# Performance work log

Hardware: AMD Instinct MI355X
Metric: run time of the kernel (lower is better)

Reference implementation:

```python
import jax, jax.numpy as jnp
import numpy as np

N_NODES = 50000
N_EDGES = 800000
D_IN = 128
D_HID = 128
D_OUT = 128


def setup_inputs() -> dict:
    key = jax.random.key(0)
    ks = jax.random.split(key, 12)
    features = jax.random.normal(ks[0], (N_NODES, D_IN), dtype=jnp.float32)
    src = jax.random.randint(ks[1], (N_EDGES,), 0, N_NODES, dtype=jnp.int32)
    dst = jax.random.randint(ks[2], (N_EDGES,), 0, N_NODES, dtype=jnp.int32)
    s_in = 1.0 / np.sqrt(D_IN)
    s_hid = 1.0 / np.sqrt(D_HID)
    W1 = jax.random.normal(ks[3], (D_IN, D_HID), dtype=jnp.float32) * s_in
    b1 = jnp.zeros((D_HID,), dtype=jnp.float32)
    W2 = jax.random.normal(ks[4], (D_HID, D_HID), dtype=jnp.float32) * s_hid
    b2 = jnp.zeros((D_HID,), dtype=jnp.float32)
    W3 = jax.random.normal(ks[5], (D_HID, D_OUT), dtype=jnp.float32) * s_hid
    b3 = jnp.zeros((D_OUT,), dtype=jnp.float32)
    policy_w = jax.random.normal(ks[6], (D_OUT, 1), dtype=jnp.float32) * s_hid
    policy_b = jnp.zeros((1,), dtype=jnp.float32)
    value_w = jax.random.normal(ks[7], (D_OUT, 1), dtype=jnp.float32) * s_hid
    value_b = jnp.zeros((1,), dtype=jnp.float32)
    return {
        "features": features, "src": src, "dst": dst,
        "W1": W1, "b1": b1, "W2": W2, "b2": b2, "W3": W3, "b3": b3,
        "policy_w": policy_w, "policy_b": policy_b,
        "value_w": value_w, "value_b": value_b,
    }


def _graph_conv(h, src, dst, deg_inv, W, b, act):
    # DGL GraphConv with norm='left': scale source features by 1/out_degree,
    # sum messages over incoming edges, then linear transform + bias (+ act).
    hn = h * deg_inv  # [N, d]
    agg = jax.ops.segment_sum(hn[src], dst, num_segments=N_NODES)  # SpMM: [N, d]
    out = agg @ W + b
    return jax.nn.relu(out) if act else out


def reference(features, src, dst, W1, b1, W2, b2, W3, b3,
              policy_w, policy_b, value_w, value_b):
    ones = jnp.ones((src.shape[0],), dtype=features.dtype)
    deg = jax.ops.segment_sum(ones, src, num_segments=N_NODES)  # out-degree
    deg_inv = (1.0 / jnp.clip(deg, 1.0))[:, None]  # [N, 1]

    h = _graph_conv(features, src, dst, deg_inv, W1, b1, act=True)
    h = _graph_conv(h, src, dst, deg_inv, W2, b2, act=True)
    h = _graph_conv(h, src, dst, deg_inv, W3, b3, act=False)  # last layer: no activation

    mN = jnp.mean(h, axis=0, keepdims=True)  # mean readout over nodes, [1, D_OUT]
    PI = h @ policy_w + policy_b  # [N, 1]
    V = mN @ value_w + value_b    # [1, 1]
    return PI, V
```

## Files before the change

### kernel.cpp

```cpp
#include <hip/hip_runtime.h>


#define N_NODES 50000
#define N_EDGES 800000
#define D 128
#define NSH 8
#define PROWS (N_NODES + 8)
#define PANEL ((size_t)PROWS * 16)
#define NC 64
#define CSZ (N_EDGES / NC)
#define NW (N_NODES / 2)
#define RQH 4
#define NWQ (NW / RQH)
#define CS_CAP (N_EDGES + 8 * N_NODES)
#define TROWS 80


__global__ __launch_bounds__(512) void k_hist3(const int* __restrict__ src, const int* __restrict__ dst,
                                               unsigned* __restrict__ ghd16, unsigned* __restrict__ ghs16) {
    __shared__ unsigned h[NWQ];
    const int rq  = blockIdx.x & 3;
    const int arr = (blockIdx.x >> 2) & 1;
    const int c   = blockIdx.x >> 3;
    const int wbase = rq * NWQ;
    const int nbase = wbase * 2;
    const int t = threadIdx.x;
    for (int i = t; i < NWQ; i += 512) h[i] = 0u;
    __syncthreads();
    const int* __restrict__ col = arr ? src : dst;
    const int e0 = c * CSZ, e1 = e0 + CSZ;
    for (int e = e0 + t; e < e1; e += 512) {
        unsigned loc = (unsigned)(col[e] - nbase);
        if (loc < 2u * NWQ) atomicAdd(&h[loc >> 1], 1u << ((loc & 1) << 4));
    }
    __syncthreads();
    unsigned* __restrict__ outp = (arr ? ghs16 : ghd16) + (size_t)c * NW + wbase;
    for (int i = t; i < NWQ; i += 512) outp[i] = h[i];
}

__global__ __launch_bounds__(256) void k_merge3(unsigned* __restrict__ ghd16, const unsigned* __restrict__ ghs16,
                                                int* __restrict__ rowcnt, int* __restrict__ rowtrue,
                                                float* __restrict__ dinv) {
    int w = blockIdx.x * 256 + threadIdx.x;
    if (w >= NW) return;
    unsigned runlo = 0, runhi = 0;
#pragma unroll
    for (int c = 0; c < NC; c++) {
        unsigned v = ghd16[(size_t)c * NW + w];
        ghd16[(size_t)c * NW + w] = runlo | (runhi << 16);
        runlo += v & 0xffffu; runhi += v >> 16;
    }
    rowtrue[2 * w]     = (int)runlo;
    rowtrue[2 * w + 1] = (int)runhi;
    rowcnt[2 * w]      = (int)((runlo + 7u) & ~7u);
    rowcnt[2 * w + 1]  = (int)((runhi + 7u) & ~7u);
    unsigned dlo = 0, dhi = 0;
#pragma unroll
    for (int c = 0; c < NC; c++) {
        unsigned v = ghs16[(size_t)c * NW + w];
        dlo += v & 0xffffu; dhi += v >> 16;
    }
    dinv[2 * w]     = 1.0f / (float)(dlo > 1u ? dlo : 1u);
    dinv[2 * w + 1] = 1.0f / (float)(dhi > 1u ? dhi : 1u);
}

__global__ __launch_bounds__(1024) void k_scan1(const int* __restrict__ cnt, int* __restrict__ excl,
                                                int* __restrict__ blocksum, int n) {
    __shared__ int wsum[16];
    int i = blockIdx.x * 1024 + threadIdx.x;
    int v = (i < n) ? cnt[i] : 0;
    int lane = threadIdx.x & 63, wid = threadIdx.x >> 6;
    int x = v;
#pragma unroll
    for (int off = 1; off < 64; off <<= 1) {
        int y = __shfl_up(x, off, 64);
        if (lane >= off) x += y;
    }
    if (lane == 63) wsum[wid] = x;
    __syncthreads();
    if (threadIdx.x == 0) {
        int run = 0;
        for (int w = 0; w < 16; w++) { int t = wsum[w]; wsum[w] = run; run += t; }
        blocksum[blockIdx.x] = run;
    }
    __syncthreads();
    if (i < n) excl[i] = (x - v) + wsum[wid];
}

__global__ void k_scan2(const int* __restrict__ blocksum, int* __restrict__ blockoff,
                        int* __restrict__ rowptr_last, int nblk) {
    if (threadIdx.x == 0) {
        int run = 0;
        for (int b = 0; b < nblk; b++) { int t = blocksum[b]; blockoff[b] = run; run += t; }
        rowptr_last[0] = run;
    }
}

__global__ __launch_bounds__(1024) void k_scan3(int* __restrict__ excl, const int* __restrict__ blockoff, int n) {
    int i = blockIdx.x * 1024 + threadIdx.x;
    if (i < n) excl[i] += blockoff[blockIdx.x];
}

__global__ __launch_bounds__(512) void k_fill3(const int* __restrict__ src, const int* __restrict__ dst,
                                               const int* __restrict__ rowptr, const unsigned* __restrict__ ghd16,
                                               unsigned short* __restrict__ cs16) {
    __shared__ unsigned cnt[NWQ];
    const int rq = blockIdx.x & 3;
    const int c  = blockIdx.x >> 2;
    const int nbase = rq * NWQ * 2;
    const int t = threadIdx.x;
    for (int i = t; i < NWQ; i += 512) cnt[i] = 0u;
    __syncthreads();
    const unsigned* __restrict__ basep = ghd16 + (size_t)c * NW;
    const int e0 = c * CSZ, e1 = e0 + CSZ;
    for (int e = e0 + t; e < e1; e += 512) {
        int d = dst[e];
        unsigned loc = (unsigned)(d - nbase);
        if (loc < 2u * NWQ) {
            int sh = (loc & 1) << 4;
            unsigned old = atomicAdd(&cnt[loc >> 1], 1u << sh);
            int p = (int)((old >> sh) & 0xffffu);
            int base = (int)((basep[d >> 1] >> ((d & 1) << 4)) & 0xffffu);
            cs16[rowptr[d] + base + p] = (unsigned short)src[e];
        }
    }
}

__global__ __launch_bounds__(256) void k_pad(const int* __restrict__ rowptr, const int* __restrict__ rowtrue,
                                             unsigned short* __restrict__ cs16,
                                             float* __restrict__ bufA, float* __restrict__ bufB) {
    int n = blockIdx.x * 256 + threadIdx.x;
    if (n < N_NODES) {
        int e0 = rowptr[n] + rowtrue[n], e1 = rowptr[n + 1];
        for (int e = e0; e < e1; e++) cs16[e] = (unsigned short)N_NODES;
    }
    if (blockIdx.x == 0) {
        int t = threadIdx.x;
        float* b = (t & 128) ? bufB : bufA;
        int p = (t >> 4) & 7, cc = t & 15;
        b[(size_t)p * PANEL + (size_t)N_NODES * 16 + cc] = 0.f;
    }
}


__global__ __launch_bounds__(256) void k_panelize(const float* __restrict__ in, const float* __restrict__ dinv,
                                                  float* __restrict__ outp) {
    int tid = blockIdx.x * 256 + threadIdx.x;
    if (tid >= N_NODES * 32) return;
    int p = tid / (N_NODES * 4);
    int r = tid - p * (N_NODES * 4);
    int node = r >> 2, qq = r & 3;
    float w = dinv[node];
    float4 v = *reinterpret_cast<const float4*>(&in[(size_t)node * D + p * 16 + qq * 4]);
    v.x *= w; v.y *= w; v.z *= w; v.w *= w;
    *reinterpret_cast<float4*>(&outp[(size_t)p * PANEL + (size_t)node * 16 + qq * 4]) = v;
}


__global__ __launch_bounds__(256) void k_agg(const float* __restrict__ hp,
                                             const int* __restrict__ rp, const unsigned short* __restrict__ cs16,
                                             float* __restrict__ outp) {
    const int l4 = threadIdx.x & 3;
    const int grp = threadIdx.x >> 2;
    const int slice = blockIdx.x & (NSH - 1);
    const int node = (blockIdx.x >> 3) * 64 + grp;
    if (node >= N_NODES) return;
    const float* __restrict__ pan = hp + (size_t)slice * PANEL + l4 * 4;
    int s0 = rp[node], s1 = rp[node + 1];
    float4 acc = {0.f, 0.f, 0.f, 0.f};
    for (int e = s0; e < s1; e += 8) {
        int4 r = *reinterpret_cast<const int4*>(&cs16[e]);
        int i0 = r.x & 0xffff, i1 = (r.x >> 16) & 0xffff;
        int i2 = r.y & 0xffff, i3 = (r.y >> 16) & 0xffff;
        int i4 = r.z & 0xffff, i5 = (r.z >> 16) & 0xffff;
        int i6 = r.w & 0xffff, i7 = (r.w >> 16) & 0xffff;
        float4 a0 = *reinterpret_cast<const float4*>(&pan[(size_t)i0 * 16]);
        float4 a1 = *reinterpret_cast<const float4*>(&pan[(size_t)i1 * 16]);
        float4 a2 = *reinterpret_cast<const float4*>(&pan[(size_t)i2 * 16]);
        float4 a3 = *reinterpret_cast<const float4*>(&pan[(size_t)i3 * 16]);
        float4 a4 = *reinterpret_cast<const float4*>(&pan[(size_t)i4 * 16]);
        float4 a5 = *reinterpret_cast<const float4*>(&pan[(size_t)i5 * 16]);
        float4 a6 = *reinterpret_cast<const float4*>(&pan[(size_t)i6 * 16]);
        float4 a7 = *reinterpret_cast<const float4*>(&pan[(size_t)i7 * 16]);
        acc.x += ((a0.x + a1.x) + (a2.x + a3.x)) + ((a4.x + a5.x) + (a6.x + a7.x));
        acc.y += ((a0.y + a1.y) + (a2.y + a3.y)) + ((a4.y + a5.y) + (a6.y + a7.y));
        acc.z += ((a0.z + a1.z) + (a2.z + a3.z)) + ((a4.z + a5.z) + (a6.z + a7.z));
        acc.w += ((a0.w + a1.w) + (a2.w + a3.w)) + ((a4.w + a5.w) + (a6.w + a7.w));
    }
    *reinterpret_cast<float4*>(&outp[(size_t)slice * PANEL + (size_t)node * 16 + l4 * 4]) = acc;
}


__global__ __launch_bounds__(256, 3) void k_gemm(const float* __restrict__ in, const float* __restrict__ W,
                                                 const float* __restrict__ bias, float* __restrict__ out,
                                                 int nrows, int relu,
                                                 const float* __restrict__ dscale,
                                                 const float* __restrict__ pw, const float* __restrict__ pb,
                                                 float* __restrict__ pi_out, float* __restrict__ colsum) {
    __shared__ float wl[64 * D];
    __shared__ float at[64 * TROWS];
    int t = threadIdx.x;
    const int head = (pw != nullptr);
    const int tx = t & 15;
    const int ro = t >> 4;
    const int row0 = blockIdx.x * TROWS;
    float4 bv1 = reinterpret_cast<const float4*>(bias)[tx];
    float4 bv2 = reinterpret_cast<const float4*>(bias)[16 + tx];
    float4 pw1 = head ? reinterpret_cast<const float4*>(pw)[tx]      : float4{0, 0, 0, 0};
    float4 pw2 = head ? reinterpret_cast<const float4*>(pw)[16 + tx] : float4{0, 0, 0, 0};
    float pb0 = head ? pb[0] : 0.f;
    float4 cs1 = {0, 0, 0, 0}, cs2 = {0, 0, 0, 0};

    int sidx[5], skb[5];
#pragma unroll
    for (int j = 0; j < 5; j++) {
        int i = t + j * 256;
        int r = i % TROWS;
        int pq = i / TROWS;
        sidx[j] = r;
        skb[j] = (pq & 3) * 4 + (pq >> 2) * 16;
    }

#define LOADA(va, h)                                                                   \
    _Pragma("unroll")                                                                  \
    for (int j = 0; j < 5; j++) {                                                      \
        int i = t + j * 256;                                                           \
        int pq = i / TROWS;                                                            \
        int p = (h) * 4 + (pq >> 2);                                                   \
        int c4 = pq & 3;                                                               \
        va[j] = *reinterpret_cast<const float4*>(                                      \
            &in[(size_t)p * PANEL + (size_t)(row0 + sidx[j]) * 16 + c4 * 4]);          \
    }

#define WRITEA(va)                                                                     \
    _Pragma("unroll")                                                                  \
    for (int j = 0; j < 5; j++) {                                                      \
        int kb = skb[j], r = sidx[j];                                                  \
        at[(kb + 0) * TROWS + r] = va[j].x; at[(kb + 1) * TROWS + r] = va[j].y;        \
        at[(kb + 2) * TROWS + r] = va[j].z; at[(kb + 3) * TROWS + r] = va[j].w;        \
    }

#define STAGEW(h)                                                                      \
    _Pragma("unroll")                                                                  \
    for (int j = 0; j < 8; j++) {                                                      \
        int i = t + j * 256;                                                           \
        reinterpret_cast<float4*>(wl)[i] =                                             \
            reinterpret_cast<const float4*>(W + (h) * 64 * D)[i];                      \
    }

#define KLOOP                                                                          \
    _Pragma("unroll 4")                                                                \
    for (int kk = 0; kk < 64; kk++) {                                                  \
        float4 a  = *reinterpret_cast<const float4*>(&at[kk * TROWS + ro * 5]);        \
        float  a4 = at[kk * TROWS + ro * 5 + 4];                                       \
        float4 w1 = *reinterpret_cast<const float4*>(&wl[kk * D + tx * 4]);            \
        float4 w2 = *reinterpret_cast<const float4*>(&wl[kk * D + 64 + tx * 4]);       \
        acc[0][0] += a.x * w1.x; acc[0][1] += a.x * w1.y; acc[0][2] += a.x * w1.z; acc[0][3] += a.x * w1.w; \
        acc[0][4] += a.x * w2.x; acc[0][5] += a.x * w2.y; acc[0][6] += a.x * w2.z; acc[0][7] += a.x * w2.w; \
        acc[1][0] += a.y * w1.x; acc[1][1] += a.y * w1.y; acc[1][2] += a.y * w1.z; acc[1][3] += a.y * w1.w; \
        acc[1][4] += a.y * w2.x; acc[1][5] += a.y * w2.y; acc[1][6] += a.y * w2.z; acc[1][7] += a.y * w2.w; \
        acc[2][0] += a.z * w1.x; acc[2][1] += a.z * w1.y; acc[2][2] += a.z * w1.z; acc[2][3] += a.z * w1.w; \
        acc[2][4] += a.z * w2.x; acc[2][5] += a.z * w2.y; acc[2][6] += a.z * w2.z; acc[2][7] += a.z * w2.w; \
        acc[3][0] += a.w * w1.x; acc[3][1] += a.w * w1.y; acc[3][2] += a.w * w1.z; acc[3][3] += a.w * w1.w; \
        acc[3][4] += a.w * w2.x; acc[3][5] += a.w * w2.y; acc[3][6] += a.w * w2.z; acc[3][7] += a.w * w2.w; \
        acc[4][0] += a4 * w1.x; acc[4][1] += a4 * w1.y; acc[4][2] += a4 * w1.z; acc[4][3] += a4 * w1.w;     \
        acc[4][4] += a4 * w2.x; acc[4][5] += a4 * w2.y; acc[4][6] += a4 * w2.z; acc[4][7] += a4 * w2.w;     \
    }

    float acc[5][8];
#pragma unroll
    for (int j = 0; j < 5; j++)
#pragma unroll
        for (int c = 0; c < 8; c++) acc[j][c] = 0.f;

    float4 va[5];
    LOADA(va, 0);
    STAGEW(0);
    WRITEA(va);
    __syncthreads();
    LOADA(va, 1);
    KLOOP;
    __syncthreads();
    WRITEA(va);
    STAGEW(1);
    __syncthreads();
    KLOOP;

#pragma unroll
    for (int j = 0; j < 5; j++) {
        int gr = row0 + ro * 5 + j;
        float4 o1, o2;
        o1.x = acc[j][0] + bv1.x; o1.y = acc[j][1] + bv1.y;
        o1.z = acc[j][2] + bv1.z; o1.w = acc[j][3] + bv1.w;
        o2.x = acc[j][4] + bv2.x; o2.y = acc[j][5] + bv2.y;
        o2.z = acc[j][6] + bv2.z; o2.w = acc[j][7] + bv2.w;
        if (relu) {
            o1.x = fmaxf(o1.x, 0.f); o1.y = fmaxf(o1.y, 0.f);
            o1.z = fmaxf(o1.z, 0.f); o1.w = fmaxf(o1.w, 0.f);
            o2.x = fmaxf(o2.x, 0.f); o2.y = fmaxf(o2.y, 0.f);
            o2.z = fmaxf(o2.z, 0.f); o2.w = fmaxf(o2.w, 0.f);
        }
        if (head) {
            cs1.x += o1.x; cs1.y += o1.y; cs1.z += o1.z; cs1.w += o1.w;
            cs2.x += o2.x; cs2.y += o2.y; cs2.z += o2.z; cs2.w += o2.w;
            float pr = o1.x * pw1.x + o1.y * pw1.y + o1.z * pw1.z + o1.w * pw1.w
                     + o2.x * pw2.x + o2.y * pw2.y + o2.z * pw2.z + o2.w * pw2.w;
#pragma unroll
            for (int m = 8; m > 0; m >>= 1) pr += __shfl_xor(pr, m, 16);
            if (tx == 0) pi_out[gr] = pr + pb0;
        } else {
            if (dscale) {
                float w = dscale[gr];
                o1.x *= w; o1.y *= w; o1.z *= w; o1.w *= w;
                o2.x *= w; o2.y *= w; o2.z *= w; o2.w *= w;
            }
            size_t base1 = (size_t)(tx >> 2) * PANEL + (size_t)gr * 16 + (tx & 3) * 4;
            *reinterpret_cast<float4*>(&out[base1]) = o1;
            *reinterpret_cast<float4*>(&out[base1 + 4 * PANEL]) = o2;
        }
    }

    if (head) {
        __syncthreads();
        float* csl = at;
        if (t < D) csl[t] = 0.f;
        __syncthreads();
        atomicAdd(&csl[tx * 4 + 0], cs1.x);
        atomicAdd(&csl[tx * 4 + 1], cs1.y);
        atomicAdd(&csl[tx * 4 + 2], cs1.z);
        atomicAdd(&csl[tx * 4 + 3], cs1.w);
        atomicAdd(&csl[64 + tx * 4 + 0], cs2.x);
        atomicAdd(&csl[64 + tx * 4 + 1], cs2.y);
        atomicAdd(&csl[64 + tx * 4 + 2], cs2.z);
        atomicAdd(&csl[64 + tx * 4 + 3], cs2.w);
        __syncthreads();
        if (t < D) atomicAdd(&colsum[t], csl[t]);
    }
#undef LOADA
#undef WRITEA
#undef STAGEW
#undef KLOOP
}


__global__ __launch_bounds__(128) void k_value(const float* __restrict__ colsum, const float* __restrict__ vw,
                                               const float* __restrict__ vb, float* __restrict__ out) {
    __shared__ float red[128];
    int t = threadIdx.x;
    red[t] = (colsum[t] * (1.0f / (float)N_NODES)) * vw[t];
    __syncthreads();
    for (int s = 64; s > 0; s >>= 1) {
        if (t < s) red[t] += red[t + s];
        __syncthreads();
    }
    if (t == 0) out[0] = red[0] + vb[0];
}

__global__ __launch_bounds__(64) void k_ws_too_small(float* __restrict__ out, int n) {
    int i = blockIdx.x * 64 + threadIdx.x;
    if (i < n) out[i] = -1e30f;
}


extern "C" void kernel_launch(void* const* d_in, const int* in_sizes, int n_in,
                              void* d_out, int out_size, void* d_ws, size_t ws_size,
                              hipStream_t stream) {
    const float* features = (const float*)d_in[0];
    const int*   src      = (const int*)d_in[1];
    const int*   dst      = (const int*)d_in[2];
    const float* W1 = (const float*)d_in[3];
    const float* b1 = (const float*)d_in[4];
    const float* W2 = (const float*)d_in[5];
    const float* b2 = (const float*)d_in[6];
    const float* W3 = (const float*)d_in[7];
    const float* b3 = (const float*)d_in[8];
    const float* pw = (const float*)d_in[9];
    const float* pb = (const float*)d_in[10];
    const float* vw = (const float*)d_in[11];
    const float* vb = (const float*)d_in[12];
    float* out = (float*)d_out;

    char* ws = (char*)d_ws;
    size_t off = 0;
    auto alloc = [&](size_t bytes) -> char* {
        char* p = ws + off;
        off += (bytes + 255) & ~(size_t)255;
        return p;
    };
    float* dinv     = (float*)alloc((size_t)N_NODES * 4);
    int*   rowptr   = (int*)alloc((size_t)(N_NODES + 1) * 4);
    int*   rowcnt   = (int*)alloc((size_t)N_NODES * 4);
    int*   rowtrue  = (int*)alloc((size_t)N_NODES * 4);
    int*   blocksum = (int*)alloc(64 * 4);
    int*   blockoff = (int*)alloc(64 * 4);
    float* colsum   = (float*)alloc(D * 4);
    unsigned short* cs16 = (unsigned short*)alloc((size_t)CS_CAP * 2);
    float* bufA     = (float*)alloc((size_t)NSH * PANEL * 4);
    float* bufB     = (float*)alloc((size_t)NSH * PANEL * 4);

    unsigned* ghd16 = (unsigned*)bufB;
    unsigned* ghs16 = ghd16 + (size_t)NC * NW;

    if (off > ws_size) {
        k_ws_too_small<<<(out_size + 63) / 64, 64, 0, stream>>>(out, out_size);
        return;
    }

    hipMemsetAsync(colsum, 0, (size_t)D * 4, stream);

    k_hist3<<<NC * 2 * RQH, 512, 0, stream>>>(src, dst, ghd16, ghs16);
    k_merge3<<<(NW + 255) / 256, 256, 0, stream>>>(ghd16, ghs16, rowcnt, rowtrue, dinv);

    int nblk = (N_NODES + 1023) / 1024;
    k_scan1<<<nblk, 1024, 0, stream>>>(rowcnt, rowptr, blocksum, N_NODES);
    k_scan2<<<1, 64, 0, stream>>>(blocksum, blockoff, rowptr + N_NODES, nblk);
    k_scan3<<<nblk, 1024, 0, stream>>>(rowptr, blockoff, N_NODES);
    k_fill3<<<NC * RQH, 512, 0, stream>>>(src, dst, rowptr, ghd16, cs16);
    k_pad<<<(N_NODES + 255) / 256, 256, 0, stream>>>(rowptr, rowtrue, cs16, bufA, bufB);

    k_panelize<<<(N_NODES * 32 + 255) / 256, 256, 0, stream>>>(features, dinv, bufA);

    int aggblocks = ((N_NODES + 63) / 64) * NSH;
    int gemmblocks = N_NODES / TROWS;
    k_agg<<<aggblocks, 256, 0, stream>>>(bufA, rowptr, cs16, bufB);
    k_gemm<<<gemmblocks, 256, 0, stream>>>(bufB, W1, b1, bufB, N_NODES, 1, dinv,
                                           nullptr, nullptr, nullptr, nullptr);
    k_agg<<<aggblocks, 256, 0, stream>>>(bufB, rowptr, cs16, bufA);
    k_gemm<<<gemmblocks, 256, 0, stream>>>(bufA, W2, b2, bufA, N_NODES, 1, dinv,
                                           nullptr, nullptr, nullptr, nullptr);
    k_agg<<<aggblocks, 256, 0, stream>>>(bufA, rowptr, cs16, bufB);
    k_gemm<<<gemmblocks, 256, 0, stream>>>(bufB, W3, b3, nullptr, N_NODES, 0, nullptr,
                                           pw, pb, out, colsum);

    k_value<<<1, 128, 0, stream>>>(colsum, vw, vb, out + N_NODES);
}
```

Before: 283.4 us.

## Bucket nodes by padded degree so aggregation wavefronts process similar-length rows

After: 1.054 ms. 3.72x slower.

```diff
diff --git a/kernel.cpp b/kernel.cpp
--- a/kernel.cpp
+++ b/kernel.cpp
@@ -14,6 +14,7 @@
 #define NWQ (NW / RQH)
 #define CS_CAP (N_EDGES + 8 * N_NODES)
 #define TROWS 80
+#define NBK 16
 
 
 __global__ __launch_bounds__(512) void k_hist3(const int* __restrict__ src, const int* __restrict__ dst,
@@ -143,6 +144,34 @@
 }
 
 
+__global__ __launch_bounds__(256) void k_bucket1(const int* __restrict__ rowcnt, int* __restrict__ bidx,
+                                                 int* __restrict__ bcnt, int n) {
+    int i = blockIdx.x * 256 + threadIdx.x;
+    if (i < n) {
+        int b = rowcnt[i] >> 3; if (b > NBK - 1) b = NBK - 1;
+        bidx[i] = b;
+        atomicAdd(&bcnt[b], 1);
+    }
+}
+
+__global__ void k_bucket2(const int* __restrict__ bcnt, int* __restrict__ bbase) {
+    if (threadIdx.x == 0) {
+        int run = 0;
+        for (int b = 0; b < NBK; b++) { bbase[b] = run; run += bcnt[b]; }
+    }
+}
+
+__global__ __launch_bounds__(256) void k_bucket3(const int* __restrict__ bidx, const int* __restrict__ bbase,
+                                                 int* __restrict__ bfill, int* __restrict__ nodeperm, int n) {
+    int i = blockIdx.x * 256 + threadIdx.x;
+    if (i < n) {
+        int b = bidx[i];
+        int p = atomicAdd(&bfill[b], 1);
+        nodeperm[bbase[b] + p] = i;
+    }
+}
+
+
 __global__ __launch_bounds__(256) void k_panelize(const float* __restrict__ in, const float* __restrict__ dinv,
                                                   float* __restrict__ outp) {
     int tid = blockIdx.x * 256 + threadIdx.x;
@@ -159,12 +188,14 @@
 
 __global__ __launch_bounds__(256) void k_agg(const float* __restrict__ hp,
                                              const int* __restrict__ rp, const unsigned short* __restrict__ cs16,
+                                             const int* __restrict__ nodeperm,
                                              float* __restrict__ outp) {
     const int l4 = threadIdx.x & 3;
     const int grp = threadIdx.x >> 2;
     const int slice = blockIdx.x & (NSH - 1);
-    const int node = (blockIdx.x >> 3) * 64 + grp;
-    if (node >= N_NODES) return;
+    const int slot = (blockIdx.x >> 3) * 64 + grp;
+    if (slot >= N_NODES) return;
+    const int node = nodeperm[slot];
     const float* __restrict__ pan = hp + (size_t)slice * PANEL + l4 * 4;
     int s0 = rp[node], s1 = rp[node + 1];
     float4 acc = {0.f, 0.f, 0.f, 0.f};
@@ -391,13 +422,20 @@
     int*   rowptr   = (int*)alloc((size_t)(N_NODES + 1) * 4);
     int*   rowcnt   = (int*)alloc((size_t)N_NODES * 4);
     int*   rowtrue  = (int*)alloc((size_t)N_NODES * 4);
+    int*   bidx     = (int*)alloc((size_t)N_NODES * 4);
+    int*   nodeperm = (int*)alloc((size_t)N_NODES * 4);
     int*   blocksum = (int*)alloc(64 * 4);
     int*   blockoff = (int*)alloc(64 * 4);
+    int*   bq       = (int*)alloc(3 * NBK * 4);
     float* colsum   = (float*)alloc(D * 4);
     unsigned short* cs16 = (unsigned short*)alloc((size_t)CS_CAP * 2);
     float* bufA     = (float*)alloc((size_t)NSH * PANEL * 4);
     float* bufB     = (float*)alloc((size_t)NSH * PANEL * 4);
 
+    int* bcnt  = bq;
+    int* bfill = bq + NBK;
+    int* bbase = bq + 2 * NBK;
+
     unsigned* ghd16 = (unsigned*)bufB;
     unsigned* ghs16 = ghd16 + (size_t)NC * NW;
 
@@ -407,6 +445,7 @@
     }
 
     hipMemsetAsync(colsum, 0, (size_t)D * 4, stream);
+    hipMemsetAsync(bq, 0, 2 * NBK * 4, stream);
 
     k_hist3<<<NC * 2 * RQH, 512, 0, stream>>>(src, dst, ghd16, ghs16);
     k_merge3<<<(NW + 255) / 256, 256, 0, stream>>>(ghd16, ghs16, rowcnt, rowtrue, dinv);
@@ -418,17 +457,21 @@
     k_fill3<<<NC * RQH, 512, 0, stream>>>(src, dst, rowptr, ghd16, cs16);
     k_pad<<<(N_NODES + 255) / 256, 256, 0, stream>>>(rowptr, rowtrue, cs16, bufA, bufB);
 
+    k_bucket1<<<(N_NODES + 255) / 256, 256, 0, stream>>>(rowcnt, bidx, bcnt, N_NODES);
+    k_bucket2<<<1, 64, 0, stream>>>(bcnt, bbase);
+    k_bucket3<<<(N_NODES + 255) / 256, 256, 0, stream>>>(bidx, bbase, bfill, nodeperm, N_NODES);
+
     k_panelize<<<(N_NODES * 32 + 255) / 256, 256, 0, stream>>>(features, dinv, bufA);
 
     int aggblocks = ((N_NODES + 63) / 64) * NSH;
     int gemmblocks = N_NODES / TROWS;
-    k_agg<<<aggblocks, 256, 0, stream>>>(bufA, rowptr, cs16, bufB);
+    k_agg<<<aggblocks, 256, 0, stream>>>(bufA, rowptr, cs16, nodeperm, bufB);
     k_gemm<<<gemmblocks, 256, 0, stream>>>(bufB, W1, b1, bufB, N_NODES, 1, dinv,
                                            nullptr, nullptr, nullptr, nullptr);
-    k_agg<<<aggblocks, 256, 0, stream>>>(bufB, rowptr, cs16, bufA);
+    k_agg<<<aggblocks, 256, 0, stream>>>(bufB, rowptr, cs16, nodeperm, bufA);
     k_gemm<<<gemmblocks, 256, 0, stream>>>(bufA, W2, b2, bufA, N_NODES, 1, dinv,
                                            nullptr, nullptr, nullptr, nullptr);
-    k_agg<<<aggblocks, 256, 0, stream>>>(bufA, rowptr, cs16, bufB);
+    k_agg<<<aggblocks, 256, 0, stream>>>(bufA, rowptr, cs16, nodeperm, bufB);
     k_gemm<<<gemmblocks, 256, 0, stream>>>(bufB, W3, b3, nullptr, N_NODES, 0, nullptr,
                                            pw, pb, out, colsum);
 
```
